# Performance work log

Hardware: AMD Instinct MI355X
Metric: run time of the kernel (lower is better)

## Reference

```python
import jax, jax.numpy as jnp
import numpy as np


def _ln(x, g, b, eps=1e-5):
    m = x.mean(-1, keepdims=True)
    v = ((x - m) ** 2).mean(-1, keepdims=True)
    return (x - m) / jnp.sqrt(v + eps) * g + b


def _conv(x, w, b, stride, pad, groups):
    # x: NCHW, w: OIHW (I = in_ch/groups)
    out = jax.lax.conv_general_dilated(
        x, w, (stride, stride), [(pad, pad), (pad, pad)],
        dimension_numbers=('NCHW', 'OIHW', 'NCHW'), feature_group_count=groups)
    return out + b[None, :, None, None]


def _gelu(x):
    return jax.nn.gelu(x, approximate=False)  # torch nn.GELU (exact erf)


def _forward(x, H, W, lpu_w, lpu_b, n1_g, n1_b, conv2d_w, conv2d_b, cn_g, cn_b,
             q_w, sr1_w, sr1_b, an1_g, an1_b, sr2_w, sr2_b, an2_g, an2_b,
             kv1_w, kv2_w, proj_w, proj_b, n2_g, n2_b,
             fc1_w, fc1_b, dw_w, dw_b, fc2_w, fc2_b):
    B, N, C = x.shape
    cd = C // 4          # conv_part_dim = 64
    ad = C - cd          # attn_part_dim = 192
    nh = 8
    hg = nh // 2         # heads per group
    hd = ad // nh        # head_dim = 24
    scale = hd ** -0.5
    # ---- LPU: depthwise 3x3 conv residual ----
    xi = x.transpose(0, 2, 1).reshape(B, C, H, W)
    xi = _conv(xi, lpu_w, lpu_b, 1, 1, C) + xi
    x = xi.reshape(B, C, N).transpose(0, 2, 1)
    # ---- Attention branch (pre-LN) ----
    y = _ln(x, n1_g, n1_b)
    cp, ap = y[..., :cd], y[..., cd:]
    # conv part: dense 3x3 conv (sr_ratio==8 -> kernel 3, pad 1), then LN+GELU in NLC
    cp = cp.reshape(B, H, W, cd).transpose(0, 3, 1, 2)
    cp = _conv(cp, conv2d_w, conv2d_b, 1, 1, 1).reshape(B, cd, N).transpose(0, 2, 1)
    cp = _gelu(_ln(cp, cn_g, cn_b))
    # attn part: dual spatial-reduction KV paths
    q = (ap @ q_w.T).reshape(B, N, nh, hd).transpose(0, 2, 1, 3)  # [B,nh,N,hd]
    x_ = ap.transpose(0, 2, 1).reshape(B, ad, H, W)
    x1 = _conv(x_, sr1_w, sr1_b, 8, 0, ad).reshape(B, ad, -1).transpose(0, 2, 1)  # [B,(H/8)(W/8),ad]
    x1 = _gelu(_ln(x1, an1_g, an1_b))
    x2 = _conv(x_, sr2_w, sr2_b, 4, 0, ad).reshape(B, ad, -1).transpose(0, 2, 1)  # [B,(H/4)(W/4),ad]
    x2 = _gelu(_ln(x2, an2_g, an2_b))
    kv1 = (x1 @ kv1_w.T).reshape(B, -1, 2, hg, hd).transpose(2, 0, 3, 1, 4)  # [2,B,hg,M1,hd]
    kv2 = (x2 @ kv2_w.T).reshape(B, -1, 2, hg, hd).transpose(2, 0, 3, 1, 4)

    def attn(qh, k, v):
        a = jax.nn.softmax(jnp.einsum('bhnd,bhmd->bhnm', qh, k) * scale, axis=-1)
        o = jnp.einsum('bhnm,bhmd->bhnd', a, v)
        return o.transpose(0, 2, 1, 3).reshape(B, N, -1)

    o1 = attn(q[:, :hg], kv1[0], kv1[1])
    o2 = attn(q[:, hg:], kv2[0], kv2[1])
    y = jnp.concatenate([o1, o2, cp], axis=-1) @ proj_w.T + proj_b
    x = x + y
    # ---- MLP with depthwise conv ----
    z = _ln(x, n2_g, n2_b) @ fc1_w.T + fc1_b
    hidc = z.shape[-1]
    z = z.transpose(0, 2, 1).reshape(B, hidc, H, W)
    z = _conv(z, dw_w, dw_b, 1, 1, hidc).reshape(B, hidc, N).transpose(0, 2, 1)
    z = _gelu(z) @ fc2_w.T + fc2_b
    return x + z


def setup_inputs() -> dict:
    key = jax.random.key(0)
    ks = jax.random.split(key, 16)
    B, H, W, C = 16, 56, 56, 256
    N = H * W
    cd, ad = C // 4, C * 3 // 4
    hid = 4 * C
    f = lambda i, shape, s=0.02: jax.random.normal(ks[i], shape, jnp.float32) * s
    return dict(
        x=jax.random.normal(ks[0], (B, N, C), jnp.float32),
        H=H, W=W,
        lpu_w=f(1, (C, 1, 3, 3), 0.1), lpu_b=jnp.zeros((C,), jnp.float32),
        n1_g=jnp.ones((C,), jnp.float32), n1_b=jnp.zeros((C,), jnp.float32),
        conv2d_w=f(2, (cd, cd, 3, 3), 0.05), conv2d_b=jnp.zeros((cd,), jnp.float32),
        cn_g=jnp.ones((cd,), jnp.float32), cn_b=jnp.zeros((cd,), jnp.float32),
        q_w=f(3, (ad, ad)),
        sr1_w=f(4, (ad, 1, 8, 8), 0.1), sr1_b=jnp.zeros((ad,), jnp.float32),
        an1_g=jnp.ones((ad,), jnp.float32), an1_b=jnp.zeros((ad,), jnp.float32),
        sr2_w=f(5, (ad, 1, 4, 4), 0.1), sr2_b=jnp.zeros((ad,), jnp.float32),
        an2_g=jnp.ones((ad,), jnp.float32), an2_b=jnp.zeros((ad,), jnp.float32),
        kv1_w=f(6, (ad, ad)), kv2_w=f(7, (ad, ad)),
        proj_w=f(8, (C, C)), proj_b=jnp.zeros((C,), jnp.float32),
        n2_g=jnp.ones((C,), jnp.float32), n2_b=jnp.zeros((C,), jnp.float32),
        fc1_w=f(9, (hid, C)), fc1_b=jnp.zeros((hid,), jnp.float32),
        dw_w=f(10, (hid, 1, 3, 3), 0.1), dw_b=jnp.zeros((hid,), jnp.float32),
        fc2_w=f(11, (C, hid)), fc2_b=jnp.zeros((C,), jnp.float32),
    )


def reference(x, H, W, lpu_w, lpu_b, n1_g, n1_b, conv2d_w, conv2d_b, cn_g, cn_b,
              q_w, sr1_w, sr1_b, an1_g, an1_b, sr2_w, sr2_b, an2_g, an2_b,
              kv1_w, kv2_w, proj_w, proj_b, n2_g, n2_b,
              fc1_w, fc1_b, dw_w, dw_b, fc2_w, fc2_b):
    return _forward(x, H, W, lpu_w, lpu_b, n1_g, n1_b, conv2d_w, conv2d_b, cn_g, cn_b,
                    q_w, sr1_w, sr1_b, an1_g, an1_b, sr2_w, sr2_b, an2_g, an2_b,
                    kv1_w, kv2_w, proj_w, proj_b, n2_g, n2_b,
                    fc1_w, fc1_b, dw_w, dw_b, fc2_w, fc2_b)
```

## Files before the change

### kernel.cpp

```cpp
#include <hip/hip_runtime.h>
#include <math.h>

#define BB   16
#define HH   56
#define WW   56
#define NN   (HH*WW)
#define CC   256
#define CD   64
#define AD   192
#define NH   8
#define HG   4
#define HD   24
#define HID  1024
#define M1   49
#define M2   196
#define BNR  (BB*NN)

typedef __attribute__((ext_vector_type(8))) short s8v;
typedef __attribute__((ext_vector_type(4))) short s4v;
typedef __attribute__((ext_vector_type(4))) float f4v;
typedef __attribute__((ext_vector_type(8))) _Float16 h8v;
typedef __attribute__((ext_vector_type(2))) _Float16 h2v;

__device__ __forceinline__ float gelu_f(float x) {
    float u = x * (1.0f + 0.044715f * x * x);
    float t = __expf(-1.5957691216f * u);
    return x * __builtin_amdgcn_rcpf(1.0f + t);
}
__device__ __forceinline__ ushort f2bf(float f) {
    union { float f; uint32_t u; } c; c.f = f;
    uint32_t u = c.u;
    return (ushort)((u + 0x7fffu + ((u >> 16) & 1u)) >> 16);
}
__device__ __forceinline__ float bf2f(ushort u) {
    union { uint32_t u; float f; } c; c.u = ((uint32_t)u) << 16;
    return c.f;
}
__device__ __forceinline__ ushort f2h(float f) {
    union { _Float16 h; ushort u; } c; c.h = (_Float16)f;
    return c.u;
}
__device__ __forceinline__ void load_lds16(const void* gsrc, void* ldst) {
    __builtin_amdgcn_global_load_lds(
        (const __attribute__((address_space(1))) void*)gsrc,
        (__attribute__((address_space(3))) void*)ldst, 16, 0, 0);
}
__device__ __forceinline__ int xcd_swz(int bid, int nwg) {
    int q = nwg >> 3, r = nwg & 7;
    int x = bid & 7, i = bid >> 3;
    return (x < r ? x * (q + 1) : r * (q + 1) + (x - r) * q) + i;
}

__global__ __launch_bounds__(256) void wprep_kernel(
        const float* __restrict__ qw, const float* __restrict__ k1,
        const float* __restrict__ k2, const float* __restrict__ pw,
        const float* __restrict__ f1, const float* __restrict__ f2,
        const float* __restrict__ cw, const float* __restrict__ lw,
        const float* __restrict__ dw,
        ushort* __restrict__ wq, ushort* __restrict__ wkv1,
        ushort* __restrict__ wkv2, ushort* __restrict__ wpr,
        ushort* __restrict__ wf1, ushort* __restrict__ wf2,
        ushort* __restrict__ wcp, float* __restrict__ lpwt,
        ushort* __restrict__ dwwth) {
    int i = blockIdx.x * 256 + threadIdx.x;
    if (i < 36864) { wq[i] = f2bf(qw[i]); return; } i -= 36864;
    if (i < 36864) { wkv1[i] = f2bf(k1[i]); return; } i -= 36864;
    if (i < 36864) { wkv2[i] = f2bf(k2[i]); return; } i -= 36864;
    if (i < 65536) { wpr[i] = f2bf(pw[i]); return; } i -= 65536;
    if (i < 262144) { wf1[i] = f2bf(f1[i]); return; } i -= 262144;
    if (i < 262144) { wf2[i] = f2h(f2[i]); return; } i -= 262144;
    if (i < 36864) {
        int co = i / 576, k = i - co * 576;
        int tap = k >> 6, ci = k & 63;
        wcp[i] = f2bf(cw[co * 576 + ci * 9 + tap]);
        return;
    } i -= 36864;
    if (i < 2304) { int c = i / 9, t = i - c * 9; lpwt[t * CC + c] = lw[i]; return; } i -= 2304;
    if (i < 9216) { int c = i / 9, t = i - c * 9; dwwth[t * HID + c] = f2h(dw[i]); }
}

__global__ __launch_bounds__(256) void lpu_kernel(const float* __restrict__ x,
        const float* __restrict__ wt, const float* __restrict__ bias,
        const float* __restrict__ n1g, const float* __restrict__ n1b,
        ushort* __restrict__ xbuf, ushort* __restrict__ ybuf) {
    int tid = threadIdx.x;
    int lane = tid & 63, wv = tid >> 6;
    int c = lane * 4;
    int grp = xcd_swz(blockIdx.x, NN / 16) * 4 + wv;
    int n0 = grp * 4;
    int h = n0 / WW, x0 = n0 - h * WW;
    int b = blockIdx.y;
    const float* xb = x + (size_t)b * NN * CC + c;
    float4 wreg[9];
#pragma unroll
    for (int t = 0; t < 9; ++t) wreg[t] = *(const float4*)(wt + t * CC + c);
    float4 bz = *(const float4*)(bias + c);
    float4 acc[4] = {bz, bz, bz, bz};
#pragma unroll
    for (int cx = 0; cx < 6; ++cx) {
        int wx = x0 + cx - 1;
        if ((unsigned)wx >= (unsigned)WW) continue;
#pragma unroll
        for (int ky = 0; ky < 3; ++ky) {
            int hy = h + ky - 1;
            if ((unsigned)hy >= (unsigned)HH) continue;
            float4 xv = *(const float4*)(xb + (size_t)(hy * WW + wx) * CC);
#pragma unroll
            for (int xo = 0; xo < 4; ++xo) {
                int kx = cx - xo;
                if (kx < 0 || kx > 2) continue;
                float4 wv4 = wreg[ky * 3 + kx];
                acc[xo].x = fmaf(xv.x, wv4.x, acc[xo].x);
                acc[xo].y = fmaf(xv.y, wv4.y, acc[xo].y);
                acc[xo].z = fmaf(xv.z, wv4.z, acc[xo].z);
                acc[xo].w = fmaf(xv.w, wv4.w, acc[xo].w);
            }
        }
    }
    float4 gv = *(const float4*)(n1g + c);
    float4 bv = *(const float4*)(n1b + c);
#pragma unroll
    for (int xo = 0; xo < 4; ++xo) {
        size_t o = ((size_t)b * NN + n0 + xo) * CC + c;
        float4 rv = *(const float4*)(x + o);
        float4 a = acc[xo];
        a.x += rv.x; a.y += rv.y; a.z += rv.z; a.w += rv.w;
        s4v xv4;
        xv4.x = (short)f2bf(a.x);
        xv4.y = (short)f2bf(a.y);
        xv4.z = (short)f2bf(a.z);
        xv4.w = (short)f2bf(a.w);
        *(s4v*)(xbuf + o) = xv4;
        float s = a.x + a.y + a.z + a.w;
        float sq = a.x * a.x + a.y * a.y + a.z * a.z + a.w * a.w;
#pragma unroll
        for (int off = 32; off >= 1; off >>= 1) {
            s += __shfl_xor(s, off, 64);
            sq += __shfl_xor(sq, off, 64);
        }
        float mean = s * (1.0f / 256.0f);
        float var = sq * (1.0f / 256.0f) - mean * mean;
        float rstd = rsqrtf(var + 1e-5f);
        s4v ov;
        ov.x = (short)f2bf((a.x - mean) * rstd * gv.x + bv.x);
        ov.y = (short)f2bf((a.y - mean) * rstd * gv.y + bv.y);
        ov.z = (short)f2bf((a.z - mean) * rstd * gv.z + bv.z);
        ov.w = (short)f2bf((a.w - mean) * rstd * gv.w + bv.w);
        *(s4v*)(ybuf + o) = ov;
    }
}

__global__ __launch_bounds__(256) void cpgemm_kernel(
        const ushort* __restrict__ y, const ushort* __restrict__ wt,
        const float* __restrict__ cb, const float* __restrict__ cng,
        const float* __restrict__ cnb, ushort* __restrict__ cat) {
    __shared__ __align__(16) ushort As[128 * 32];
    __shared__ __align__(16) ushort Ws[64 * 32];
    int tid = threadIdx.x;
    int wid = tid >> 6, lane = tid & 63;
    int rt = xcd_swz(blockIdx.x, BNR / 128) * 128;
    int r0 = tid >> 2, c0 = tid & 3;
    int r1 = r0 + 64;
    int tok0 = rt + r0, tok1 = rt + r1;
    int b0 = tok0 / NN, n0 = tok0 - b0 * NN, h0 = n0 / WW, w0 = n0 - h0 * WW;
    int b1 = tok1 / NN, n1 = tok1 - b1 * NN, h1 = n1 / WW, w1 = n1 - h1 * WW;
    const ushort* Wp = wt + (size_t)r0 * 576 + c0 * 8;
    int aw0 = (c0 ^ (r0 & 3)) << 3;
    f4v acc[2][4];
#pragma unroll
    for (int m = 0; m < 2; ++m)
#pragma unroll
        for (int n = 0; n < 4; ++n) acc[m][n] = (f4v)0.f;
    int lr = lane & 15, g4 = lane >> 4;
    int swz = (g4 ^ (lr & 3)) << 3;
    for (int kt = 0; kt < 576; kt += 32) {
        int tap = kt >> 6, ci0 = kt & 63;
        int t3 = tap / 3, dy = t3 - 1, dx = (tap - t3 * 3) - 1;
        s8v a0 = (s8v)0, a1 = (s8v)0;
        int hy0 = h0 + dy, wx0 = w0 + dx;
        if ((unsigned)hy0 < (unsigned)HH && (unsigned)wx0 < (unsigned)WW)
            a0 = *(const s8v*)(y + ((size_t)b0 * NN + hy0 * WW + wx0) * CC + ci0 + c0 * 8);
        int hy1 = h1 + dy, wx1 = w1 + dx;
        if ((unsigned)hy1 < (unsigned)HH && (unsigned)wx1 < (unsigned)WW)
            a1 = *(const s8v*)(y + ((size_t)b1 * NN + hy1 * WW + wx1) * CC + ci0 + c0 * 8);
        s8v wv = *(const s8v*)(Wp + kt);
        __syncthreads();
        *(s8v*)&As[r0 * 32 + aw0] = a0;
        *(s8v*)&As[r1 * 32 + aw0] = a1;
        *(s8v*)&Ws[r0 * 32 + aw0] = wv;
        __syncthreads();
        s8v af[2], bf[4];
#pragma unroll
        for (int m = 0; m < 2; ++m)
            af[m] = *(const s8v*)&As[(wid * 32 + m * 16 + lr) * 32 + swz];
#pragma unroll
        for (int n = 0; n < 4; ++n)
            bf[n] = *(const s8v*)&Ws[(n * 16 + lr) * 32 + swz];
#pragma unroll
        for (int m = 0; m < 2; ++m)
#pragma unroll
            for (int n = 0; n < 4; ++n)
                acc[m][n] = __builtin_amdgcn_mfma_f32_16x16x32_bf16(af[m], bf[n], acc[m][n], 0, 0, 0);
    }
    float gv[4], bv[4], cbv[4];
#pragma unroll
    for (int n = 0; n < 4; ++n) {
        int gc = n * 16 + lr;
        cbv[n] = cb[gc];
        gv[n] = cng[gc];
        bv[n] = cnb[gc];
    }
#pragma unroll
    for (int m = 0; m < 2; ++m)
#pragma unroll
        for (int r = 0; r < 4; ++r) {
            float s = 0.f, sq = 0.f;
#pragma unroll
            for (int n = 0; n < 4; ++n) {
                float v = acc[m][n][r] + cbv[n];
                acc[m][n][r] = v;
                s += v; sq += v * v;
            }
#pragma unroll
            for (int off = 1; off < 16; off <<= 1) {
                s += __shfl_xor(s, off, 64);
                sq += __shfl_xor(sq, off, 64);
            }
            float mean = s * (1.0f / 64.0f);
            float var = sq * (1.0f / 64.0f) - mean * mean;
            float rstd = rsqrtf(var + 1e-5f);
            int row = rt + wid * 32 + m * 16 + g4 * 4 + r;
            ushort* op = cat + (size_t)row * CC + 192;
#pragma unroll
            for (int n = 0; n < 4; ++n) {
                float v = (acc[m][n][r] - mean) * rstd * gv[n] + bv[n];
                op[n * 16 + lr] = f2bf(gelu_f(v));
            }
        }
}

template <int KS, int OW>
__global__ __launch_bounds__(192) void sr_kernel(const ushort* __restrict__ yap,
        const float* __restrict__ w, const float* __restrict__ bias,
        const float* __restrict__ g, const float* __restrict__ bt,
        ushort* __restrict__ out) {
    int ch = threadIdx.x;
    int m = blockIdx.x, b = blockIdx.y;
    int oh = m / OW, ow = m - oh * OW;
    const ushort* yb = yap + (size_t)b * NN * CC;
    float acc = bias[ch];
#pragma unroll
    for (int ky = 0; ky < KS; ++ky)
#pragma unroll
        for (int kx = 0; kx < KS; ++kx)
            acc = fmaf(bf2f(yb[(size_t)((oh * KS + ky) * WW + ow * KS + kx) * CC + ch]),
                       w[ch * KS * KS + ky * KS + kx], acc);
    __shared__ float red[2][3];
    float s = acc, sq = acc * acc;
#pragma unroll
    for (int off = 32; off >= 1; off >>= 1) {
        s += __shfl_xor(s, off, 64);
        sq += __shfl_xor(sq, off, 64);
    }
    int wv = threadIdx.x >> 6, lane = threadIdx.x & 63;
    if (lane == 0) { red[0][wv] = s; red[1][wv] = sq; }
    __syncthreads();
    s = red[0][0] + red[0][1] + red[0][2];
    sq = red[1][0] + red[1][1] + red[1][2];
    float mean = s * (1.0f / 192.0f);
    float var = sq * (1.0f / 192.0f) - mean * mean;
    float rstd = rsqrtf(var + 1e-5f);
    float v = (acc - mean) * rstd * g[ch] + bt[ch];
    out[((size_t)b * (OW * OW) + m) * AD + ch] = f2bf(gelu_f(v));
}

template <int MODE, int F16 = 0>
__global__ __launch_bounds__(512) void gemm_mfma(
        const ushort* __restrict__ A, int lda,
        const ushort* __restrict__ W, int K, int O,
        const float* __restrict__ bias,
        const ushort* __restrict__ res, int ldr,
        void* __restrict__ Cout, int ldc, int R) {
    __shared__ __align__(16) ushort As[2 * 256 * 32];
    __shared__ __align__(16) ushort Ws[2 * 128 * 32];
    int tid = threadIdx.x;
    int w8 = tid >> 6, lane = tid & 63;
    int wr = w8 >> 1, wc = w8 & 1;
    int nwg = gridDim.x * gridDim.y;
    int swzb = xcd_swz(blockIdx.y * gridDim.x + blockIdx.x, nwg);
    int rt = (swzb / gridDim.x) * 256, ot = (swzb % gridDim.x) * 128;
    int r0 = tid >> 2, cslot = tid & 3;
    int csrc = (cslot ^ (r0 & 3)) * 8;
    const ushort* Ap0 = A + (size_t)min(rt + r0, R - 1) * lda + csrc;
    const ushort* Ap1 = A + (size_t)min(rt + r0 + 128, R - 1) * lda + csrc;
    const ushort* Wp0 = W + (size_t)min(ot + r0, O - 1) * K + csrc;
    char* lA0 = (char*)As + w8 * 1024;
    char* lA1 = (char*)As + 8192 + w8 * 1024;
    char* lW0 = (char*)Ws + w8 * 1024;
    f4v acc[4][4];
#pragma unroll
    for (int m = 0; m < 4; ++m)
#pragma unroll
        for (int n = 0; n < 4; ++n) acc[m][n] = (f4v)0.f;
    int lr = lane & 15;
    int swz = ((lane >> 4) ^ (lr & 3)) << 3;
    load_lds16(Ap0, lA0);
    load_lds16(Ap1, lA1);
    load_lds16(Wp0, lW0);
    __syncthreads();
    int cur = 0;
    for (int kt = 0; kt < K; kt += 32) {
        if (kt + 32 < K) {
            int pa = (cur ^ 1) * 16384, pw = (cur ^ 1) * 8192;
            load_lds16(Ap0 + kt + 32, lA0 + pa);
            load_lds16(Ap1 + kt + 32, lA1 + pa);
            load_lds16(Wp0 + kt + 32, lW0 + pw);
        }
        const ushort* Ab = As + cur * 8192;
        const ushort* Wb = Ws + cur * 4096;
        s8v af[4], bf[4];
#pragma unroll
        for (int m = 0; m < 4; ++m)
            af[m] = *(const s8v*)&Ab[(wr * 64 + m * 16 + lr) * 32 + swz];
#pragma unroll
        for (int n = 0; n < 4; ++n)
            bf[n] = *(const s8v*)&Wb[(wc * 64 + n * 16 + lr) * 32 + swz];
#pragma unroll
        for (int m = 0; m < 4; ++m)
#pragma unroll
            for (int n = 0; n < 4; ++n) {
                if (F16) {
                    h8v ah = *(const h8v*)&af[m];
                    h8v bh = *(const h8v*)&bf[n];
                    acc[m][n] = __builtin_amdgcn_mfma_f32_16x16x32_f16(ah, bh, acc[m][n], 0, 0, 0);
                } else {
                    acc[m][n] = __builtin_amdgcn_mfma_f32_16x16x32_bf16(af[m], bf[n], acc[m][n], 0, 0, 0);
                }
            }
        __syncthreads();
        cur ^= 1;
    }
#pragma unroll
    for (int m = 0; m < 4; ++m)
#pragma unroll
        for (int n = 0; n < 4; ++n) {
            int gr = rt + wr * 64 + m * 16 + (lane >> 4) * 4;
            int gc = ot + wc * 64 + n * 16 + (lane & 15);
            if (gc >= O) continue;
#pragma unroll
            for (int r = 0; r < 4; ++r) {
                int row = gr + r;
                if (row >= R) continue;
                float v = acc[m][n][r];
                if (MODE & 1) v += bias[gc];
                if (MODE & 2) v += bf2f(res[(size_t)row * ldr + gc]);
                if (MODE & 4)      ((ushort*)Cout)[(size_t)row * ldc + gc] = f2bf(v);
                else if (MODE & 8) ((ushort*)Cout)[(size_t)row * ldc + gc] = f2h(v);
                else               ((float*)Cout)[(size_t)row * ldc + gc] = v;
            }
        }
}

__global__ __launch_bounds__(512) void projln_kernel(
        const ushort* __restrict__ A, const ushort* __restrict__ W,
        const float* __restrict__ bias,
        const float* __restrict__ n2g, const float* __restrict__ n2b,
        ushort* __restrict__ xbuf, ushort* __restrict__ ybuf) {
    __shared__ __align__(16) ushort As[128 * 32];
    __shared__ __align__(16) ushort Ws[256 * 32];
    int tid = threadIdx.x;
    int w8 = tid >> 6, lane = tid & 63;
    int rt = xcd_swz(blockIdx.x, BNR / 128) * 128;
    int r0 = tid >> 2, cslot = tid & 3;
    int csrc = (cslot ^ (r0 & 3)) * 8;
    const ushort* Ap0 = A + (size_t)(rt + r0) * CC + csrc;
    const ushort* Wp0 = W + (size_t)r0 * CC + csrc;
    const ushort* Wp1 = W + (size_t)(r0 + 128) * CC + csrc;
    char* lA0 = (char*)As + w8 * 1024;
    char* lW0 = (char*)Ws + w8 * 1024;
    char* lW1 = (char*)Ws + 8192 + w8 * 1024;
    int lr = lane & 15, g4 = lane >> 4;
    int swz = (g4 ^ (lr & 3)) << 3;
    f4v acc[16];
#pragma unroll
    for (int n = 0; n < 16; ++n) acc[n] = (f4v)(bias[n * 16 + lr]);
    for (int kt = 0; kt < CC; kt += 32) {
        __syncthreads();
        load_lds16(Ap0 + kt, lA0);
        load_lds16(Wp0 + kt, lW0);
        load_lds16(Wp1 + kt, lW1);
        __syncthreads();
        s8v af = *(const s8v*)&As[(w8 * 16 + lr) * 32 + swz];
#pragma unroll
        for (int n = 0; n < 16; ++n) {
            s8v bf = *(const s8v*)&Ws[(n * 16 + lr) * 32 + swz];
            acc[n] = __builtin_amdgcn_mfma_f32_16x16x32_bf16(af, bf, acc[n], 0, 0, 0);
        }
    }
#pragma unroll
    for (int r = 0; r < 4; ++r) {
        int row = rt + w8 * 16 + g4 * 4 + r;
        ushort* xr = xbuf + (size_t)row * CC;
        ushort* yr = ybuf + (size_t)row * CC;
        float s = 0.f, sq = 0.f;
#pragma unroll
        for (int n = 0; n < 16; ++n) {
            float v = acc[n][r] + bf2f(xr[n * 16 + lr]);
            acc[n][r] = v;
            s += v; sq += v * v;
        }
#pragma unroll
        for (int off = 1; off < 16; off <<= 1) {
            s += __shfl_xor(s, off, 64);
            sq += __shfl_xor(sq, off, 64);
        }
        float mean = s * (1.0f / 256.0f);
        float var = sq * (1.0f / 256.0f) - mean * mean;
        float rstd = rsqrtf(var + 1e-5f);
#pragma unroll
        for (int n = 0; n < 16; ++n) {
            int col = n * 16 + lr;
            float v = acc[n][r];
            xr[col] = f2bf(v);
            yr[col] = f2bf((v - mean) * rstd * n2g[col] + n2b[col]);
        }
    }
}

template <int M, int MP, int HOFF>
__global__ __launch_bounds__(256) void attn_mfma(const ushort* __restrict__ q,
        const ushort* __restrict__ kvb, ushort* __restrict__ cat) {
    constexpr int NT = MP / 16;
    constexpr int NCH = MP / 32;
    __shared__ __align__(16) ushort Kl[MP * 32];
    __shared__ __align__(16) ushort VT[32 * MP];
    int g = blockIdx.y, b = blockIdx.z;
    int h = HOFF + g;
    int tid = threadIdx.x;
    for (int i = tid; i < MP * 4; i += 256) ((s8v*)Kl)[i] = (s8v)0;
    for (int i = tid; i < MP * 4; i += 256) ((s8v*)VT)[i] = (s8v)0;
    __syncthreads();
    for (int u = tid; u < M * 3; u += 256) {
        int m = u / 3, d0 = u - m * 3;
        s8v kv8 = *(const s8v*)(kvb + ((size_t)b * M + m) * AD + g * HD + d0 * 8);
        *(s8v*)&Kl[m * 32 + ((d0 ^ (m & 3)) << 3)] = kv8;
    }
    for (int u = tid; u < M * 3; u += 256) {
        int m = u / 3, d0 = u - m * 3;
        s8v vv = *(const s8v*)(kvb + ((size_t)b * M + m) * AD + 96 + g * HD + d0 * 8);
        int c = m >> 5, mm = m & 31;
        int gg = (mm >> 2) & 3;
        int t = (mm & 3) + ((mm & 16) >> 2);
#pragma unroll
        for (int j = 0; j < 8; ++j) {
            int d = d0 * 8 + j;
            VT[d * MP + ((c * 4 + (gg ^ (d & 3))) << 3) + t] = (ushort)vv[j];
        }
    }
    __syncthreads();
    int w = tid >> 6, lane = tid & 63;
    int ln = lane & 15, g4 = lane >> 4;
    int swz = (g4 ^ (ln & 3)) << 3;
    const float scale = 0.20412414523193154f;
    for (int nt = 0; nt < 4; ++nt) {
        int nbase = blockIdx.x * 256 + nt * 64;
        if (nbase >= NN) break;
        int n0 = nbase + w * 16 + ln;
        s8v qf = (s8v)0;
        if (g4 < 3) qf = *(const s8v*)(q + ((size_t)b * NN + n0) * AD + h * HD + g4 * 8);
        f4v sa[NT];
#pragma unroll
        for (int t = 0; t < NT; ++t) sa[t] = (f4v)0.f;
#pragma unroll
        for (int t = 0; t < NT; ++t) {
            s8v kf = *(const s8v*)&Kl[(t * 16 + ln) * 32 + swz];
            sa[t] = __builtin_amdgcn_mfma_f32_16x16x32_bf16(kf, qf, sa[t], 0, 0, 0);
        }
        float mx = -3.0e38f;
#pragma unroll
        for (int t = 0; t < NT; ++t)
#pragma unroll
            for (int r = 0; r < 4; ++r) {
                int m = t * 16 + g4 * 4 + r;
                float v = (m < M) ? sa[t][r] * scale : -3.0e38f;
                sa[t][r] = v;
                mx = fmaxf(mx, v);
            }
        mx = fmaxf(mx, __shfl_xor(mx, 16, 64));
        mx = fmaxf(mx, __shfl_xor(mx, 32, 64));
        float sum = 0.f;
#pragma unroll
        for (int t = 0; t < NT; ++t)
#pragma unroll
            for (int r = 0; r < 4; ++r) {
                float p = __expf(sa[t][r] - mx);
                sa[t][r] = p;
                sum += p;
            }
        sum += __shfl_xor(sum, 16, 64);
        sum += __shfl_xor(sum, 32, 64);
        float inv = 1.0f / sum;
        f4v oa[2] = {(f4v)0.f, (f4v)0.f};
#pragma unroll
        for (int c = 0; c < NCH; ++c) {
            s8v pb;
#pragma unroll
            for (int t = 0; t < 4; ++t) {
                pb[t]     = (short)f2bf(sa[c * 2][t]);
                pb[4 + t] = (short)f2bf(sa[c * 2 + 1][t]);
            }
#pragma unroll
            for (int dt = 0; dt < 2; ++dt) {
                s8v vf = *(const s8v*)&VT[(dt * 16 + ln) * MP + c * 32 + swz];
                oa[dt] = __builtin_amdgcn_mfma_f32_16x16x32_bf16(vf, pb, oa[dt], 0, 0, 0);
            }
        }
        ushort* op = cat + ((size_t)b * NN + n0) * CC + h * HD;
        s4v o0;
#pragma unroll
        for (int r = 0; r < 4; ++r) o0[r] = (short)f2bf(oa[0][r] * inv);
        *(s4v*)(op + g4 * 4) = o0;
        if (g4 < 2) {
            s4v o1;
#pragma unroll
            for (int r = 0; r < 4; ++r) o1[r] = (short)f2bf(oa[1][r] * inv);
            *(s4v*)(op + 16 + g4 * 4) = o1;
        }
    }
}

__global__ __launch_bounds__(256) void dwconv_kernel(const ushort* __restrict__ z1,
        const ushort* __restrict__ wt, const float* __restrict__ bias,
        ushort* __restrict__ z2) {
    int bid = xcd_swz(blockIdx.x, HH * 7);
    int h = bid / 7, bx = bid - h * 7;
    int b = blockIdx.y;
    int c = (threadIdx.x & 127) * 8;
    int x0 = bx * 8 + (threadIdx.x >> 7) * 4;
    const ushort* zrow = z1 + ((size_t)b * NN + h * WW) * HID + c;
    h2v wreg[9][4];
#pragma unroll
    for (int t = 0; t < 9; ++t) {
        s8v w8 = *(const s8v*)(wt + t * HID + c);
        const h2v* wp = (const h2v*)&w8;
#pragma unroll
        for (int p = 0; p < 4; ++p) wreg[t][p] = wp[p];
    }
    h2v acc[4][4];
    {
        float4 b0 = *(const float4*)(bias + c);
        float4 b1 = *(const float4*)(bias + c + 4);
        h2v bz[4];
        bz[0][0] = (_Float16)b0.x; bz[0][1] = (_Float16)b0.y;
        bz[1][0] = (_Float16)b0.z; bz[1][1] = (_Float16)b0.w;
        bz[2][0] = (_Float16)b1.x; bz[2][1] = (_Float16)b1.y;
        bz[3][0] = (_Float16)b1.z; bz[3][1] = (_Float16)b1.w;
#pragma unroll
        for (int xo = 0; xo < 4; ++xo)
#pragma unroll
            for (int p = 0; p < 4; ++p) acc[xo][p] = bz[p];
    }
#pragma unroll
    for (int cx = 0; cx < 6; ++cx) {
        int wx = x0 + cx - 1;
        if ((unsigned)wx >= (unsigned)WW) continue;
#pragma unroll
        for (int ky = 0; ky < 3; ++ky) {
            int hy = h + ky - 1;
            if ((unsigned)hy >= (unsigned)HH) continue;
            s8v v = *(const s8v*)(zrow + ((size_t)(ky - 1) * WW + wx) * HID);
            const h2v* v2 = (const h2v*)&v;
#pragma unroll
            for (int xo = 0; xo < 4; ++xo) {
                int kx = cx - xo;
                if (kx < 0 || kx > 2) continue;
#pragma unroll
                for (int p = 0; p < 4; ++p)
                    acc[xo][p] = v2[p] * wreg[ky * 3 + kx][p] + acc[xo][p];
            }
        }
    }
    ushort* zo = z2 + ((size_t)b * NN + h * WW + x0) * HID + c;
#pragma unroll
    for (int xo = 0; xo < 4; ++xo) {
        s8v o;
#pragma unroll
        for (int p = 0; p < 4; ++p) {
            o[p * 2]     = (short)f2h(gelu_f((float)acc[xo][p][0]));
            o[p * 2 + 1] = (short)f2h(gelu_f((float)acc[xo][p][1]));
        }
        *(s8v*)(zo + (size_t)xo * HID) = o;
    }
}

extern "C" void kernel_launch(void* const* d_in, const int* in_sizes, int n_in,
                              void* d_out, int out_size, void* d_ws, size_t ws_size,
                              hipStream_t stream) {
    const float* x      = (const float*)d_in[0];
    const float* lpu_w  = (const float*)d_in[3];
    const float* lpu_b  = (const float*)d_in[4];
    const float* n1_g   = (const float*)d_in[5];
    const float* n1_b   = (const float*)d_in[6];
    const float* c2_w   = (const float*)d_in[7];
    const float* c2_b   = (const float*)d_in[8];
    const float* cn_g   = (const float*)d_in[9];
    const float* cn_b   = (const float*)d_in[10];
    const float* q_w    = (const float*)d_in[11];
    const float* sr1_w  = (const float*)d_in[12];
    const float* sr1_b  = (const float*)d_in[13];
    const float* an1_g  = (const float*)d_in[14];
    const float* an1_b  = (const float*)d_in[15];
    const float* sr2_w  = (const float*)d_in[16];
    const float* sr2_b  = (const float*)d_in[17];
    const float* an2_g  = (const float*)d_in[18];
    const float* an2_b  = (const float*)d_in[19];
    const float* kv1_w  = (const float*)d_in[20];
    const float* kv2_w  = (const float*)d_in[21];
    const float* proj_w = (const float*)d_in[22];
    const float* proj_b = (const float*)d_in[23];
    const float* n2_g   = (const float*)d_in[24];
    const float* n2_b   = (const float*)d_in[25];
    const float* fc1_w  = (const float*)d_in[26];
    const float* fc1_b  = (const float*)d_in[27];
    const float* dw_w   = (const float*)d_in[28];
    const float* dw_b   = (const float*)d_in[29];
    const float* fc2_w  = (const float*)d_in[30];
    const float* fc2_b  = (const float*)d_in[31];
    float* out = (float*)d_out;

    char* ws = (char*)d_ws;
    size_t off = 0;
    auto allocB = [&](size_t bytes) {
        char* p = ws + off;
        off += ((bytes + 255) & ~(size_t)255);
        return p;
    };
    ushort* xbuf = (ushort*)allocB((size_t)BNR * CC * 2);
    ushort* ybuf = (ushort*)allocB((size_t)BNR * CC * 2);
    ushort* wq   = (ushort*)allocB((size_t)AD * AD * 2);
    ushort* wkv1 = (ushort*)allocB((size_t)AD * AD * 2);
    ushort* wkv2 = (ushort*)allocB((size_t)AD * AD * 2);
    ushort* wpr  = (ushort*)allocB((size_t)CC * CC * 2);
    ushort* wf1  = (ushort*)allocB((size_t)HID * CC * 2);
    ushort* wf2  = (ushort*)allocB((size_t)CC * HID * 2);
    ushort* wcp  = (ushort*)allocB((size_t)64 * 576 * 2);
    float*  lpwt = (float*)allocB((size_t)9 * CC * 4);
    ushort* dwwt = (ushort*)allocB((size_t)9 * HID * 2);
    size_t zmark = off;
    ushort* cat  = (ushort*)allocB((size_t)BNR * CC * 2);
    ushort* qbuf = (ushort*)allocB((size_t)BNR * AD * 2);
    ushort* x1g  = (ushort*)allocB((size_t)BB * M1 * AD * 2);
    ushort* x2g  = (ushort*)allocB((size_t)BB * M2 * AD * 2);
    ushort* kv1b = (ushort*)allocB((size_t)BB * M1 * AD * 2);
    ushort* kv2b = (ushort*)allocB((size_t)BB * M2 * AD * 2);

    int CB2 = 1;
    for (int cb = 16; cb >= 1; cb >>= 1) {
        if (zmark + 2 * (size_t)cb * NN * HID * 2 <= ws_size) { CB2 = cb; break; }
    }

    dim3 b256(256), b512(512);
    wprep_kernel<<<dim3(2925), b256, 0, stream>>>(
        q_w, kv1_w, kv2_w, proj_w, fc1_w, fc2_w, c2_w, lpu_w, dw_w,
        wq, wkv1, wkv2, wpr, wf1, wf2, wcp, lpwt, dwwt);
    lpu_kernel<<<dim3(NN / 16, BB), b256, 0, stream>>>(x, lpwt, lpu_b, n1_g, n1_b, xbuf, ybuf);
    cpgemm_kernel<<<dim3(BNR / 128), b256, 0, stream>>>(ybuf, wcp, c2_b, cn_g, cn_b, cat);
    gemm_mfma<4><<<dim3(2, BNR / 256), b512, 0, stream>>>(
        ybuf + CD, CC, wq, AD, AD, nullptr, nullptr, 0, qbuf, AD, BNR);
    sr_kernel<8, 7><<<dim3(M1, BB), dim3(192), 0, stream>>>(ybuf + CD, sr1_w, sr1_b, an1_g, an1_b, x1g);
    sr_kernel<4, 14><<<dim3(M2, BB), dim3(192), 0, stream>>>(ybuf + CD, sr2_w, sr2_b, an2_g, an2_b, x2g);
    gemm_mfma<4><<<dim3(2, (BB * M1 + 255) / 256), b512, 0, stream>>>(
        x1g, AD, wkv1, AD, AD, nullptr, nullptr, 0, kv1b, AD, BB * M1);
    gemm_mfma<4><<<dim3(2, (BB * M2 + 255) / 256), b512, 0, stream>>>(
        x2g, AD, wkv2, AD, AD, nullptr, nullptr, 0, kv2b, AD, BB * M2);
    attn_mfma<M1, 64, 0><<<dim3((NN + 255) / 256, HG, BB), b256, 0, stream>>>(qbuf, kv1b, cat);
    attn_mfma<M2, 224, HG><<<dim3((NN + 255) / 256, HG, BB), b256, 0, stream>>>(qbuf, kv2b, cat);
    projln_kernel<<<dim3(BNR / 128), b512, 0, stream>>>(
        cat, wpr, proj_b, n2_g, n2_b, xbuf, ybuf);
    ushort* z1 = (ushort*)(ws + zmark);
    ushort* z2 = z1 + (size_t)CB2 * NN * HID;
    for (int c0 = 0; c0 < BB; c0 += CB2) {
        size_t tokoff = (size_t)c0 * NN;
        int Rr = CB2 * NN;
        gemm_mfma<9><<<dim3(HID / 128, (Rr + 255) / 256), b512, 0, stream>>>(
            ybuf + tokoff * CC, CC, wf1, CC, HID, fc1_b, nullptr, 0, z1, HID, Rr);
        dwconv_kernel<<<dim3(HH * 7, CB2), b256, 0, stream>>>(z1, dwwt, dw_b, z2);
        gemm_mfma<3, 1><<<dim3(CC / 128, (Rr + 255) / 256), b512, 0, stream>>>(
            z2, HID, wf2, HID, CC, fc2_b, xbuf + tokoff * CC, CC, out + tokoff * CC, CC, Rr);
    }
}
```

Measured before the change: 374.2 us.

## Add 256x256-tile GEMM with 4-stage async LDS pipeline for MLP fc1/fc2

Adds a new GEMM kernel with 256x256 output tiles, 8 waves each computing 128x64, and a multi-stage direct-to-LDS load pipeline driven by explicit vmcnt waits. It replaces the 256x128 gemm_mfma for the MLP fc1 and fc2 layers. The larger tile raises data reuse per block, and keeping several K-slices of loads in flight is meant to hide global memory latency. The kernel drops row and column bounds checks, so it assumes the row count and O are multiples of 256. It also launches fewer blocks, and the accumulator count per thread doubles, which may hurt occupancy.

```diff
diff --git a/kernel.cpp b/kernel.cpp
--- a/kernel.cpp
+++ b/kernel.cpp
@@ -359,6 +359,97 @@
                 else               ((float*)Cout)[(size_t)row * ldc + gc] = v;
             }
         }
+}
+
+template <int MODE, int F16 = 0>
+__global__ __launch_bounds__(512) void gemm_8ph(
+        const ushort* __restrict__ A, int lda,
+        const ushort* __restrict__ W, int K, int O,
+        const float* __restrict__ bias,
+        const ushort* __restrict__ res, int ldr,
+        void* __restrict__ Cout, int ldc, int R) {
+    __shared__ __align__(16) ushort Al[2 * 256 * 64];
+    __shared__ __align__(16) ushort Wl[2 * 256 * 64];
+    int tid = threadIdx.x;
+    int w8 = tid >> 6, lane = tid & 63;
+    int wr = w8 >> 2, wc = w8 & 3;
+    int nwg = gridDim.x * gridDim.y;
+    int swzb = xcd_swz(blockIdx.y * gridDim.x + blockIdx.x, nwg);
+    int rt = (swzb / gridDim.x) * 256, ot = (swzb % gridDim.x) * 256;
+    int lr = lane & 15, g4 = lane >> 4;
+    int swz = (g4 ^ (lr & 3)) << 3;
+    int ar0 = tid >> 2, sp0 = tid & 3;
+    int cs0 = ((sp0 ^ (ar0 & 3)) << 3);
+    const ushort* Ap0 = A + (size_t)(rt + ar0) * lda + cs0;
+    const ushort* Ap1 = A + (size_t)(rt + ar0 + 128) * lda + cs0;
+    const ushort* Wp0 = W + (size_t)(ot + ar0) * K + cs0;
+    const ushort* Wp1 = W + (size_t)(ot + ar0 + 128) * K + cs0;
+    int d0 = w8 * 1024;
+    int d1 = 8192 + w8 * 1024;
+    f4v acc[8][4];
+#pragma unroll
+    for (int m = 0; m < 8; ++m)
+#pragma unroll
+        for (int n = 0; n < 4; ++n)
+            acc[m][n] = (f4v)((MODE & 1) ? bias[ot + wc * 64 + n * 16 + lr] : 0.0f);
+    auto STAGE = [&](int s) {
+        int t = s >> 1, hf = s & 1;
+        int boff = (t & 1) * 32768 + hf * 16384;
+        int kc = t * 64 + hf * 32;
+        load_lds16(Ap0 + kc, (char*)Al + boff + d0);
+        load_lds16(Ap1 + kc, (char*)Al + boff + d1);
+        load_lds16(Wp0 + kc, (char*)Wl + boff + d0);
+        load_lds16(Wp1 + kc, (char*)Wl + boff + d1);
+    };
+    int nS = K >> 5;
+    STAGE(0); STAGE(1); STAGE(2);
+    for (int s = 0; s < nS; ++s) {
+        if (s < nS - 2)       asm volatile("s_waitcnt vmcnt(8)" ::: "memory");
+        else if (s == nS - 2) asm volatile("s_waitcnt vmcnt(4)" ::: "memory");
+        else                  asm volatile("s_waitcnt vmcnt(0)" ::: "memory");
+        __builtin_amdgcn_s_barrier();
+        __builtin_amdgcn_sched_barrier(0);
+        if (s + 3 < nS) STAGE(s + 3);
+        int uoff = ((s >> 1) & 1) * 16384 + (s & 1) * 8192;
+        const ushort* Ab = Al + uoff;
+        const ushort* Wb = Wl + uoff;
+        s8v af[8], bf[4];
+#pragma unroll
+        for (int m = 0; m < 8; ++m)
+            af[m] = *(const s8v*)&Ab[(wr * 128 + m * 16 + lr) * 32 + swz];
+#pragma unroll
+        for (int n = 0; n < 4; ++n)
+            bf[n] = *(const s8v*)&Wb[(wc * 64 + n * 16 + lr) * 32 + swz];
+#pragma unroll
+        for (int m = 0; m < 8; ++m)
+#pragma unroll
+            for (int n = 0; n < 4; ++n) {
+                if (F16) {
+                    h8v ah = *(const h8v*)&af[m];
+                    h8v bh = *(const h8v*)&bf[n];
+                    acc[m][n] = __builtin_amdgcn_mfma_f32_16x16x32_f16(ah, bh, acc[m][n], 0, 0, 0);
+                } else {
+                    acc[m][n] = __builtin_amdgcn_mfma_f32_16x16x32_bf16(af[m], bf[n], acc[m][n], 0, 0, 0);
+                }
+            }
+    }
+#pragma unroll
+    for (int m = 0; m < 8; ++m) {
+        int gr = rt + wr * 128 + m * 16 + g4 * 4;
+#pragma unroll
+        for (int n = 0; n < 4; ++n) {
+            int gc = ot + wc * 64 + n * 16 + lr;
+#pragma unroll
+            for (int r = 0; r < 4; ++r) {
+                int row = gr + r;
+                float v = acc[m][n][r];
+                if (MODE & 2) v += bf2f(res[(size_t)row * ldr + gc]);
+                if (MODE & 4)      ((ushort*)Cout)[(size_t)row * ldc + gc] = f2bf(v);
+                else if (MODE & 8) ((ushort*)Cout)[(size_t)row * ldc + gc] = f2h(v);
+                else               ((float*)Cout)[(size_t)row * ldc + gc] = v;
+            }
+        }
+    }
 }
 
 __global__ __launch_bounds__(512) void projln_kernel(
@@ -682,10 +773,10 @@
     for (int c0 = 0; c0 < BB; c0 += CB2) {
         size_t tokoff = (size_t)c0 * NN;
         int Rr = CB2 * NN;
-        gemm_mfma<9><<<dim3(HID / 128, (Rr + 255) / 256), b512, 0, stream>>>(
+        gemm_8ph<9><<<dim3(HID / 256, Rr / 256), b512, 0, stream>>>(
             ybuf + tokoff * CC, CC, wf1, CC, HID, fc1_b, nullptr, 0, z1, HID, Rr);
         dwconv_kernel<<<dim3(HH * 7, CB2), b256, 0, stream>>>(z1, dwwt, dw_b, z2);
-        gemm_mfma<3, 1><<<dim3(CC / 128, (Rr + 255) / 256), b512, 0, stream>>>(
+        gemm_8ph<3, 1><<<dim3(CC / 256, Rr / 256), b512, 0, stream>>>(
             z2, HID, wf2, HID, CC, fc2_b, xbuf + tokoff * CC, CC, out + tokoff * CC, CC, Rr);
     }
 }
```

New measurement: 359.6 us. -3.9%, faster.
